# Performance work log

Hardware: AMD Instinct MI355X
Metric: run time of the kernel (lower is better)

Reference implementation:

```python
import jax, jax.numpy as jnp
import numpy as np

N_NODES = 50000
N_EDGES = 600000
D_IN = 128
D_HID = 128
N_IDX = 4096


def gcn_conv(x, W, b, edge_index, num_nodes):
    """PyG GCNConv: add self loops, symmetric deg normalization, scatter-add, bias."""
    h = x @ W  # [N, D_out]
    loop = jnp.arange(num_nodes, dtype=edge_index.dtype)
    src = jnp.concatenate([edge_index[0], loop])
    dst = jnp.concatenate([edge_index[1], loop])
    deg = jax.ops.segment_sum(jnp.ones_like(dst, dtype=h.dtype), dst, num_segments=num_nodes)
    dinv = jnp.where(deg > 0, jax.lax.rsqrt(jnp.maximum(deg, 1.0)), 0.0)
    norm = dinv[src] * dinv[dst]  # [E+N]
    msgs = h[src] * norm[:, None]
    out = jax.ops.segment_sum(msgs, dst, num_segments=num_nodes)
    return out + b


def setup_inputs() -> dict:
    key = jax.random.key(0)
    ks = jax.random.split(key, 18)
    d = {
        "x": jax.random.normal(ks[0], (N_NODES, D_IN), dtype=jnp.float32),
        "syntactic_edge_index": jax.random.randint(ks[1], (2, N_EDGES), 0, N_NODES, dtype=jnp.int32),
        "sequential_edge_index": jax.random.randint(ks[2], (2, N_EDGES), 0, N_NODES, dtype=jnp.int32),
        "semantic_edge_index": jax.random.randint(ks[3], (2, N_EDGES), 0, N_NODES, dtype=jnp.int32),
        "index": jax.random.randint(ks[4], (N_IDX,), 0, N_NODES, dtype=jnp.int32),
    }
    s = 1.0 / np.sqrt(D_IN)
    names = ["syn", "seq", "sem"]
    for i, n in enumerate(names):
        d[f"w1_{n}"] = jax.random.uniform(ks[5 + i], (D_IN, D_HID), jnp.float32, -s, s)
        d[f"b1_{n}"] = jnp.zeros((D_HID,), jnp.float32)
        d[f"w2_{n}"] = jax.random.uniform(ks[8 + i], (D_HID, D_HID), jnp.float32, -s, s)
        d[f"b2_{n}"] = jnp.zeros((D_HID,), jnp.float32)
    return d


def reference(x, syntactic_edge_index, sequential_edge_index, semantic_edge_index, index,
              w1_syn, b1_syn, w1_seq, b1_seq, w1_sem, b1_sem,
              w2_syn, b2_syn, w2_seq, b2_seq, w2_sem, b2_sem):
    n = x.shape[0]
    # layer 1: three parallel GCN branches + ReLU (dropout is identity in eval mode)
    a = jax.nn.relu(gcn_conv(x, w1_syn, b1_syn, syntactic_edge_index, n))
    b = jax.nn.relu(gcn_conv(x, w1_seq, b1_seq, sequential_edge_index, n))
    c = jax.nn.relu(gcn_conv(x, w1_sem, b1_sem, semantic_edge_index, n))
    h = jnp.maximum(jnp.maximum(a, b), c)
    # layer 2
    a2 = jax.nn.relu(gcn_conv(h, w2_syn, b2_syn, syntactic_edge_index, n))
    b2 = jax.nn.relu(gcn_conv(h, w2_seq, b2_seq, sequential_edge_index, n))
    c2 = jax.nn.relu(gcn_conv(h, w2_sem, b2_sem, semantic_edge_index, n))
    out = jnp.maximum(jnp.maximum(a2, b2), c2)
    return out[index]
```

## Files before the change

kernel.cpp:

```cpp
#include <hip/hip_runtime.h>
#include <hip/hip_fp16.h>

#define NN 50000
#define NE 600000
#define NG 3
#define D  128
#define NI 4096
#define BW 1024
#define NBUCK 49
#define EPT_BIN 16
#define EPB_BIN (256 * EPT_BIN)
#define NBLK_BIN ((NE + EPB_BIN - 1) / EPB_BIN)
#define XCVT_BLKS 3125
#define WCVT_BLKS 48
#define CNT_BLKS (NBLK_BIN * NG)

typedef _Float16 half8 __attribute__((ext_vector_type(8)));
typedef _Float16 half4v __attribute__((ext_vector_type(4)));
typedef float floatx4 __attribute__((ext_vector_type(4)));

static __device__ __forceinline__ float wextract(unsigned int v) {
  unsigned short u = (unsigned short)(v >> 16);
  _Float16 h;
  __builtin_memcpy(&h, &u, 2);
  return (float)h;
}

static __device__ __forceinline__ unsigned int packsw(int s, float w) {
  _Float16 h = (_Float16)w;
  unsigned short u;
  __builtin_memcpy(&u, &h, 2);
  return (unsigned int)s | ((unsigned int)u << 16);
}


__global__ __launch_bounds__(256) void prep_kernel(
    const float* __restrict__ x, __half* __restrict__ xh,
    const float* __restrict__ W0, const float* __restrict__ W1, const float* __restrict__ W2,
    const float* __restrict__ W3, const float* __restrict__ W4, const float* __restrict__ W5,
    __half* __restrict__ Wf,
    const int* __restrict__ e0, const int* __restrict__ e1, const int* __restrict__ e2,
    int* __restrict__ bucketCnt) {
  __shared__ int cnt[NBUCK];
  int blk = blockIdx.x;
  int tid = threadIdx.x;
  if (blk < XCVT_BLKS) {
    int i = blk * 256 + tid;
    size_t base = (size_t)i * 8;
    float4 v0 = *(const float4*)&x[base];
    float4 v1 = *(const float4*)&x[base + 4];
    half8 h;
    h[0] = (_Float16)v0.x; h[1] = (_Float16)v0.y; h[2] = (_Float16)v0.z; h[3] = (_Float16)v0.w;
    h[4] = (_Float16)v1.x; h[5] = (_Float16)v1.y; h[6] = (_Float16)v1.z; h[7] = (_Float16)v1.w;
    *(half8*)&xh[base] = h;
  } else if (blk < XCVT_BLKS + WCVT_BLKS) {
    const float* Wm[6] = {W0, W1, W2, W3, W4, W5};
    int t = (blk - XCVT_BLKS) * 256 + tid;
    int mat = t >> 11;
    int fr = (t >> 6) & 31;
    int lane = t & 63;
    int tt = fr >> 2, ks = fr & 3;
    int n = tt * 16 + (lane & 15);
    int kb = ks * 32 + (lane >> 4) * 8;
    const float* W = Wm[mat];
#pragma unroll
    for (int j = 0; j < 8; j++)
      Wf[(size_t)t * 8 + j] = __float2half(W[(kb + j) * 128 + n]);
  } else {
    int cb = blk - XCVT_BLKS - WCVT_BLKS;
    int g = cb / NBLK_BIN, eb = cb % NBLK_BIN;
    const int* ei = (g == 0) ? e0 : ((g == 1) ? e1 : e2);
    if (tid < NBUCK) cnt[tid] = 0;
    __syncthreads();
    int base = eb * EPB_BIN;
#pragma unroll
    for (int i = 0; i < EPT_BIN; i++) {
      int e = base + tid + i * 256;
      if (e < NE) atomicAdd(&cnt[ei[NE + e] >> 10], 1);
    }
    __syncthreads();
    if (tid < NBUCK) atomicAdd(&bucketCnt[g * NBUCK + tid], cnt[tid]);
  }
}

__global__ void bscan_kernel(const int* __restrict__ bucketCnt, int* __restrict__ bucketBase,
                             int* __restrict__ cursor, int* __restrict__ rp) {
  int g = threadIdx.x >> 6;
  int lane = threadIdx.x & 63;
  if (g >= NG) return;
  int v = (lane < NBUCK) ? bucketCnt[g * NBUCK + lane] : 0;
  int incl = v;
#pragma unroll
  for (int off = 1; off < 64; off <<= 1) {
    int t = __shfl_up(incl, off, 64);
    if (lane >= off) incl += t;
  }
  int ex = incl - v;
  if (lane < NBUCK) {
    bucketBase[g * NBUCK + lane] = ex;
    cursor[g * NBUCK + lane] = ex;
  }
  if (lane == 0) rp[g * (NN + 1) + NN] = NE;
}

__global__ __launch_bounds__(256) void bin_kernel(const int* __restrict__ e0,
    const int* __restrict__ e1, const int* __restrict__ e2,
    int* __restrict__ cursor, unsigned int* __restrict__ binned) {
  __shared__ int cnt[4][NBUCK];
  __shared__ int base[NBUCK];
  __shared__ int woff[4][NBUCK];
  int g = blockIdx.y;
  const int* ei = (g == 0) ? e0 : ((g == 1) ? e1 : e2);
  int tid = threadIdx.x;
  int wave = tid >> 6;
  if (tid < NBUCK) { cnt[0][tid] = 0; cnt[1][tid] = 0; cnt[2][tid] = 0; cnt[3][tid] = 0; }
  __syncthreads();
  int estart = blockIdx.x * EPB_BIN;
  int src[EPT_BIN], dst[EPT_BIN], rk[EPT_BIN];
#pragma unroll
  for (int i = 0; i < EPT_BIN; i++) {
    int e = estart + tid + i * 256;
    if (e < NE) {
      src[i] = ei[e];
      dst[i] = ei[NE + e];
      rk[i] = atomicAdd(&cnt[wave][dst[i] >> 10], 1);
    } else {
      rk[i] = -1;
    }
  }
  __syncthreads();
  if (tid < NBUCK) {
    int c0 = cnt[0][tid], c1 = cnt[1][tid], c2 = cnt[2][tid], c3 = cnt[3][tid];
    int total = c0 + c1 + c2 + c3;
    base[tid] = (total > 0) ? atomicAdd(&cursor[g * NBUCK + tid], total) : 0;
    woff[0][tid] = 0; woff[1][tid] = c0; woff[2][tid] = c0 + c1; woff[3][tid] = c0 + c1 + c2;
  }
  __syncthreads();
#pragma unroll
  for (int i = 0; i < EPT_BIN; i++) {
    if (rk[i] >= 0) {
      int b = dst[i] >> 10;
      binned[(size_t)g * NE + base[b] + woff[wave][b] + rk[i]] =
          (unsigned int)src[i] | ((unsigned int)dst[i] << 16);
    }
  }
}

__global__ __launch_bounds__(256) void csr_kernel(const unsigned int* __restrict__ binned,
    const int* __restrict__ bucketBase, const int* __restrict__ bucketCnt,
    int* __restrict__ rp, float* __restrict__ dinv) {
  __shared__ int deg[BW];
  __shared__ int wsum[4];
  int g = blockIdx.y, b = blockIdx.x;
  int tid = threadIdx.x;
  int node0 = b * BW;
  int bb = bucketBase[g * NBUCK + b];
  int total = bucketCnt[g * NBUCK + b];
  const unsigned int* bp = binned + (size_t)g * NE + bb;
  for (int i = tid; i < BW; i += 256) deg[i] = 0;
  __syncthreads();
  for (int e = tid; e < total; e += 256) {
    unsigned int p = bp[e];
    atomicAdd(&deg[(int)(p >> 16) - node0], 1);
  }
  __syncthreads();
  int d0 = deg[tid * 4], d1 = deg[tid * 4 + 1], d2 = deg[tid * 4 + 2], d3 = deg[tid * 4 + 3];
  int s = d0 + d1 + d2 + d3;
  int lane = tid & 63;
  int incl = s;
#pragma unroll
  for (int off = 1; off < 64; off <<= 1) {
    int n = __shfl_up(incl, off, 64);
    if (lane >= off) incl += n;
  }
  if (lane == 63) wsum[tid >> 6] = incl;
  __syncthreads();
  int wbase = 0;
#pragma unroll
  for (int w = 0; w < 4; w++)
    if (w < (tid >> 6)) wbase += wsum[w];
  int ex = wbase + incl - s;
  int exs[4] = {ex, ex + d0, ex + d0 + d1, ex + d0 + d1 + d2};
  int ds[4] = {d0, d1, d2, d3};
#pragma unroll
  for (int k = 0; k < 4; k++) {
    int node = node0 + tid * 4 + k;
    if (node < NN) {
      rp[g * (NN + 1) + node] = bb + exs[k];
      dinv[g * NN + node] = rsqrtf((float)ds[k] + 1.0f);
    }
  }
}

__global__ __launch_bounds__(256) void fillp_kernel(const unsigned int* __restrict__ binned,
    const int* __restrict__ bucketBase, const int* __restrict__ bucketCnt,
    const int* __restrict__ rp, const float* __restrict__ dinv,
    unsigned int* __restrict__ colp) {
  __shared__ int cur[BW];
  int g = blockIdx.y, b = blockIdx.x;
  int tid = threadIdx.x;
  int node0 = b * BW;
  int bb = bucketBase[g * NBUCK + b];
  int total = bucketCnt[g * NBUCK + b];
  const unsigned int* bp = binned + (size_t)g * NE + bb;
  for (int i = tid; i < BW; i += 256) {
    int node = node0 + i;
    cur[i] = (node < NN) ? rp[g * (NN + 1) + node] : 0;
  }
  __syncthreads();
  for (int e = tid; e < total; e += 256) {
    unsigned int p = bp[e];
    int srcid = (int)(p & 0xffffu);
    int r = atomicAdd(&cur[(int)(p >> 16) - node0], 1);
    colp[(size_t)g * NE + r] = packsw(srcid, dinv[g * NN + srcid]);
  }
}


__global__ __launch_bounds__(256) void aggb_kernel(
    const __half* __restrict__ srch, const int* __restrict__ rp,
    const unsigned int* __restrict__ colp, const float* __restrict__ dinv,
    const int* __restrict__ index, __half* __restrict__ tout, int nrows) {
  int b = blockIdx.y;
  int w = (blockIdx.x * 256 + threadIdx.x) >> 6;
  if (w >= nrows) return;
  int lane = threadIdx.x & 63;
  int sub = lane >> 5;
  int fl = lane & 31;
  int node = index ? index[w] : w;
  const _Float16* srcv = (const _Float16*)srch;
  half4v selfh = *(const half4v*)&srcv[(size_t)node * D + fl * 4];
  float di = dinv[b * NN + node];
  float a[4];
#pragma unroll
  for (int k = 0; k < 4; k++) a[k] = sub ? 0.f : di * (float)selfh[k];
  const int* rpb = rp + b * (NN + 1);
  int s = rpb[node], e = rpb[node + 1];
  int n = e - s;
  const unsigned int* cp = colp + (size_t)b * NE;
  unsigned int c = (lane < n) ? cp[s + lane] : 0u;
  int m = min(n, 64);
  for (int j = 0; j < m; j += 8) {
    half4v h[4];
    float wg[4];
#pragma unroll
    for (int u = 0; u < 4; u++) {
      unsigned int v = (unsigned int)__shfl((int)c, j + u * 2 + sub, 64);
      wg[u] = wextract(v);
      h[u] = *(const half4v*)&srcv[(size_t)(v & 0xffffu) * D + fl * 4];
    }
#pragma unroll
    for (int u = 0; u < 4; u++)
#pragma unroll
      for (int k = 0; k < 4; k++) a[k] = fmaf((float)h[u][k], wg[u], a[k]);
  }
  for (int q = s + 64; q < e; q += 64) {
    int nn = min(e - q, 64);
    unsigned int cc = (lane < nn) ? cp[q + lane] : 0u;
    for (int j = 0; j < nn; j += 2) {
      unsigned int v = (unsigned int)__shfl((int)cc, j + sub, 64);
      float wf = wextract(v);
      half4v hv = *(const half4v*)&srcv[(size_t)(v & 0xffffu) * D + fl * 4];
#pragma unroll
      for (int k = 0; k < 4; k++) a[k] = fmaf((float)hv[k], wf, a[k]);
    }
  }
#pragma unroll
  for (int k = 0; k < 4; k++) a[k] += __shfl_xor(a[k], 32, 64);
  if (sub == 0) {
    half4v o;
#pragma unroll
    for (int k = 0; k < 4; k++) o[k] = (_Float16)(di * a[k]);
    _Float16* tv = (_Float16*)tout;
    *(half4v*)&tv[(size_t)b * nrows * D + (size_t)w * D + fl * 4] = o;
  }
}


#define ALD 136

__global__ __launch_bounds__(256) void mmf_kernel(const __half* __restrict__ A,
    const __half* __restrict__ Wf,
    const float* __restrict__ B0, const float* __restrict__ B1, const float* __restrict__ B2,
    __half* __restrict__ outh, float* __restrict__ outf, int M) {
  __shared__ _Float16 As[128 * ALD];
  __shared__ _Float16 Ws[16384];
  const float* Bb[3] = {B0, B1, B2};
  const int tid = threadIdx.x;
  const int wave = tid >> 6, lane = tid & 63;
  const int wr = (wave >> 1) * 64, wc = (wave & 1) * 64;
  const int ln = lane & 15, quad = lane >> 4;
  const int row0 = blockIdx.x * 128;
  float om[4][4][4];

  for (int b = 0; b < 3; b++) {
    const __half* Wb = Wf + (size_t)b * 16384;
#pragma unroll
    for (int i = 0; i < 8; i++) {
      int id = tid + i * 256;
      *(half8*)&Ws[id * 8] = *(const half8*)&Wb[(size_t)id * 8];
    }
    const __half* Ab = A + (size_t)b * M * D;
#pragma unroll
    for (int i = 0; i < 8; i++) {
      int idx = tid + i * 256;
      int r = idx >> 4, c8 = idx & 15;
      int gr = row0 + r;
      gr = (gr < M) ? gr : (M - 1);
      half8 v = *(const half8*)&Ab[(size_t)gr * D + c8 * 8];
      *(half8*)&As[r * ALD + c8 * 8] = v;
    }
    __syncthreads();

    float bias[4];
#pragma unroll
    for (int ct = 0; ct < 4; ct++) bias[ct] = Bb[b][wc + ct * 16 + ln];
    floatx4 acc[4][4];
#pragma unroll
    for (int rt = 0; rt < 4; rt++)
#pragma unroll
      for (int ct = 0; ct < 4; ct++)
        acc[rt][ct] = (floatx4){bias[ct], bias[ct], bias[ct], bias[ct]};

#pragma unroll
    for (int ks = 0; ks < 4; ks++) {
      half8 av[4];
#pragma unroll
      for (int rt = 0; rt < 4; rt++)
        av[rt] = *(const half8*)&As[(wr + rt * 16 + ln) * ALD + ks * 32 + quad * 8];
#pragma unroll
      for (int ct = 0; ct < 4; ct++) {
        int tt = (wc >> 4) + ct;
        half8 bv = *(const half8*)&Ws[((tt * 4 + ks) * 64 + lane) * 8];
#pragma unroll
        for (int rt = 0; rt < 4; rt++)
          acc[rt][ct] = __builtin_amdgcn_mfma_f32_16x16x32_f16(av[rt], bv, acc[rt][ct], 0, 0, 0);
      }
    }
#pragma unroll
    for (int rt = 0; rt < 4; rt++)
#pragma unroll
      for (int ct = 0; ct < 4; ct++)
#pragma unroll
        for (int r = 0; r < 4; r++) {
          float v = fmaxf(acc[rt][ct][r], 0.f);
          om[rt][ct][r] = (b == 0) ? v : fmaxf(om[rt][ct][r], v);
        }
    __syncthreads();
  }
#pragma unroll
  for (int rt = 0; rt < 4; rt++) {
    int m = row0 + wr + rt * 16 + quad * 4;
#pragma unroll
    for (int r = 0; r < 4; r++) {
      if (m + r < M) {
#pragma unroll
        for (int ct = 0; ct < 4; ct++) {
          int n = wc + ct * 16 + ln;
          if (outh) outh[(size_t)(m + r) * D + n] = __float2half(om[rt][ct][r]);
          else      outf[(size_t)(m + r) * D + n] = om[rt][ct][r];
        }
      }
    }
  }
}


extern "C" void kernel_launch(void* const* d_in, const int* in_sizes, int n_in,
                              void* d_out, int out_size, void* d_ws, size_t ws_size,
                              hipStream_t stream) {
  const float* x = (const float*)d_in[0];
  const int* e0 = (const int*)d_in[1];
  const int* e1 = (const int*)d_in[2];
  const int* e2 = (const int*)d_in[3];
  const int* index = (const int*)d_in[4];
  const float* w1[3] = {(const float*)d_in[5], (const float*)d_in[9],  (const float*)d_in[13]};
  const float* b1[3] = {(const float*)d_in[6], (const float*)d_in[10], (const float*)d_in[14]};
  const float* w2[3] = {(const float*)d_in[7], (const float*)d_in[11], (const float*)d_in[15]};
  const float* b2[3] = {(const float*)d_in[8], (const float*)d_in[12], (const float*)d_in[16]};
  float* out = (float*)d_out;

  char* ws = (char*)d_ws;
  size_t o = 0;
  auto alloc = [&](size_t bytes) {
    o = (o + 255) & ~(size_t)255;
    void* p = ws + o;
    o += bytes;
    return p;
  };
  int*    rp     = (int*)alloc((size_t)NG * (NN + 1) * 4);
  unsigned int* colp = (unsigned int*)alloc((size_t)NG * NE * 4);
  float*  dinv   = (float*)alloc((size_t)NG * NN * 4);
  int*    bcnt   = (int*)alloc((size_t)NG * NBUCK * 4);
  int*    bbase  = (int*)alloc((size_t)NG * NBUCK * 4);
  int*    bcur   = (int*)alloc((size_t)NG * NBUCK * 4);
  __half* xh     = (__half*)alloc((size_t)NN * D * 2);
  __half* Wf     = (__half*)alloc((size_t)6 * 128 * 128 * 2);
  __half* t1     = (__half*)alloc((size_t)NG * NN * D * 2);
  __half* hacc   = (__half*)alloc((size_t)NN * D * 2);
  unsigned int* binned = (unsigned int*)t1;
  __half* t2     = t1;
  (void)ws_size; (void)in_sizes; (void)n_in; (void)out_size;

  hipMemsetAsync(bcnt, 0, (size_t)NG * NBUCK * 4, stream);
  prep_kernel<<<XCVT_BLKS + WCVT_BLKS + CNT_BLKS, 256, 0, stream>>>(
      x, xh, w1[0], w1[1], w1[2], w2[0], w2[1], w2[2], Wf, e0, e1, e2, bcnt);
  bscan_kernel<<<1, 192, 0, stream>>>(bcnt, bbase, bcur, rp);
  bin_kernel<<<dim3(NBLK_BIN, NG), 256, 0, stream>>>(e0, e1, e2, bcur, binned);
  csr_kernel<<<dim3(NBUCK, NG), 256, 0, stream>>>(binned, bbase, bcnt, rp, dinv);
  fillp_kernel<<<dim3(NBUCK, NG), 256, 0, stream>>>(binned, bbase, bcnt, rp, dinv, colp);

  aggb_kernel<<<dim3((NN * 64 + 255) / 256, NG), 256, 0, stream>>>(
      xh, rp, colp, dinv, nullptr, t1, NN);
  mmf_kernel<<<(NN + 127) / 128, 256, 0, stream>>>(t1, Wf, b1[0], b1[1], b1[2],
                                                   hacc, nullptr, NN);
  aggb_kernel<<<dim3((NI * 64 + 255) / 256, NG), 256, 0, stream>>>(
      hacc, rp, colp, dinv, index, t2, NI);
  mmf_kernel<<<(NI + 127) / 128, 256, 0, stream>>>(t2, Wf + (size_t)3 * 16384,
                                                   b2[0], b2[1], b2[2], nullptr, out, NI);
}
```

Baseline: 279.5 us.

## Aggregate four rows per wavefront with 16-lane groups and half8 loads

Reworks the gather-aggregation kernel so each 64-lane wavefront handles four destination rows, with 16 lanes per row each loading 8 fp16 features (16-byte loads) instead of two 32-lane halves per row with 8-byte loads. Neighbor indices are fetched 16 at a time per group and broadcast by shuffle, and the final cross-half reduction is removed. The intent is to improve memory-load width and cut per-row shuffle and reduction overhead for low-degree nodes (average degree around 12). The cost is divergence: each wavefront loops to the maximum degree of its four rows, and the launch grid shrinks accordingly.

Result: no change. 275.6 us (-1.4%).

```diff
diff --git a/kernel.cpp b/kernel.cpp
--- a/kernel.cpp
+++ b/kernel.cpp
@@ -222,57 +222,60 @@
     const unsigned int* __restrict__ colp, const float* __restrict__ dinv,
     const int* __restrict__ index, __half* __restrict__ tout, int nrows) {
   int b = blockIdx.y;
-  int w = (blockIdx.x * 256 + threadIdx.x) >> 6;
-  if (w >= nrows) return;
   int lane = threadIdx.x & 63;
-  int sub = lane >> 5;
-  int fl = lane & 31;
-  int node = index ? index[w] : w;
+  int grp = lane >> 4;
+  int l16 = lane & 15;
+  int gb = grp << 4;
+  int wv = (blockIdx.x * 256 + threadIdx.x) >> 6;
+  int w = wv * 4 + grp;
+  int valid = (w < nrows);
+  int wc = valid ? w : 0;
+  int node = index ? index[wc] : wc;
   const _Float16* srcv = (const _Float16*)srch;
-  half4v selfh = *(const half4v*)&srcv[(size_t)node * D + fl * 4];
+  const int* rpb = rp + b * (NN + 1);
+  int s = rpb[node];
+  int e = rpb[node + 1];
+  int n = valid ? (e - s) : 0;
   float di = dinv[b * NN + node];
-  float a[4];
-#pragma unroll
-  for (int k = 0; k < 4; k++) a[k] = sub ? 0.f : di * (float)selfh[k];
-  const int* rpb = rp + b * (NN + 1);
-  int s = rpb[node], e = rpb[node + 1];
-  int n = e - s;
+  half8 selfh = *(const half8*)&srcv[(size_t)node * D + l16 * 8];
+  float a[8];
+#pragma unroll
+  for (int k = 0; k < 8; k++) a[k] = di * (float)selfh[k];
+  int nmax = n;
+  nmax = max(nmax, __shfl_xor(nmax, 16, 64));
+  nmax = max(nmax, __shfl_xor(nmax, 32, 64));
   const unsigned int* cp = colp + (size_t)b * NE;
-  unsigned int c = (lane < n) ? cp[s + lane] : 0u;
-  int m = min(n, 64);
-  for (int j = 0; j < m; j += 8) {
-    half4v h[4];
-    float wg[4];
-#pragma unroll
-    for (int u = 0; u < 4; u++) {
-      unsigned int v = (unsigned int)__shfl((int)c, j + u * 2 + sub, 64);
-      wg[u] = wextract(v);
-      h[u] = *(const half4v*)&srcv[(size_t)(v & 0xffffu) * D + fl * 4];
-    }
-#pragma unroll
-    for (int u = 0; u < 4; u++)
-#pragma unroll
-      for (int k = 0; k < 4; k++) a[k] = fmaf((float)h[u][k], wg[u], a[k]);
-  }
-  for (int q = s + 64; q < e; q += 64) {
-    int nn = min(e - q, 64);
-    unsigned int cc = (lane < nn) ? cp[q + lane] : 0u;
-    for (int j = 0; j < nn; j += 2) {
-      unsigned int v = (unsigned int)__shfl((int)cc, j + sub, 64);
-      float wf = wextract(v);
-      half4v hv = *(const half4v*)&srcv[(size_t)(v & 0xffffu) * D + fl * 4];
-#pragma unroll
-      for (int k = 0; k < 4; k++) a[k] = fmaf((float)hv[k], wf, a[k]);
-    }
-  }
-#pragma unroll
-  for (int k = 0; k < 4; k++) a[k] += __shfl_xor(a[k], 32, 64);
-  if (sub == 0) {
-    half4v o;
-#pragma unroll
-    for (int k = 0; k < 4; k++) o[k] = (_Float16)(di * a[k]);
+  for (int j0 = 0; j0 < nmax; j0 += 16) {
+    unsigned int c = (j0 + l16 < n) ? cp[s + j0 + l16] : 0u;
+    int rem = nmax - j0;
+    rem = (rem > 16) ? 16 : rem;
+    for (int jj = 0; jj < rem; jj += 4) {
+      unsigned int v0 = (unsigned int)__shfl((int)c, gb + jj + 0, 64);
+      unsigned int v1 = (unsigned int)__shfl((int)c, gb + jj + 1, 64);
+      unsigned int v2 = (unsigned int)__shfl((int)c, gb + jj + 2, 64);
+      unsigned int v3 = (unsigned int)__shfl((int)c, gb + jj + 3, 64);
+      half8 h0 = *(const half8*)&srcv[(size_t)(v0 & 0xffffu) * D + l16 * 8];
+      half8 h1 = *(const half8*)&srcv[(size_t)(v1 & 0xffffu) * D + l16 * 8];
+      half8 h2 = *(const half8*)&srcv[(size_t)(v2 & 0xffffu) * D + l16 * 8];
+      half8 h3 = *(const half8*)&srcv[(size_t)(v3 & 0xffffu) * D + l16 * 8];
+      float w0 = wextract(v0), w1 = wextract(v1);
+      float w2 = wextract(v2), w3 = wextract(v3);
+#pragma unroll
+      for (int k = 0; k < 8; k++) a[k] = fmaf((float)h0[k], w0, a[k]);
+#pragma unroll
+      for (int k = 0; k < 8; k++) a[k] = fmaf((float)h1[k], w1, a[k]);
+#pragma unroll
+      for (int k = 0; k < 8; k++) a[k] = fmaf((float)h2[k], w2, a[k]);
+#pragma unroll
+      for (int k = 0; k < 8; k++) a[k] = fmaf((float)h3[k], w3, a[k]);
+    }
+  }
+  if (valid) {
+    half8 o;
+#pragma unroll
+    for (int k = 0; k < 8; k++) o[k] = (_Float16)(di * a[k]);
     _Float16* tv = (_Float16*)tout;
-    *(half4v*)&tv[(size_t)b * nrows * D + (size_t)w * D + fl * 4] = o;
+    *(half8*)&tv[(size_t)b * nrows * D + (size_t)w * D + l16 * 8] = o;
   }
 }
 
@@ -410,11 +413,11 @@
   csr_kernel<<<dim3(NBUCK, NG), 256, 0, stream>>>(binned, bbase, bcnt, rp, dinv);
   fillp_kernel<<<dim3(NBUCK, NG), 256, 0, stream>>>(binned, bbase, bcnt, rp, dinv, colp);
 
-  aggb_kernel<<<dim3((NN * 64 + 255) / 256, NG), 256, 0, stream>>>(
+  aggb_kernel<<<dim3((NN + 15) / 16, NG), 256, 0, stream>>>(
       xh, rp, colp, dinv, nullptr, t1, NN);
   mmf_kernel<<<(NN + 127) / 128, 256, 0, stream>>>(t1, Wf, b1[0], b1[1], b1[2],
                                                    hacc, nullptr, NN);
-  aggb_kernel<<<dim3((NI * 64 + 255) / 256, NG), 256, 0, stream>>>(
+  aggb_kernel<<<dim3((NI + 15) / 16, NG), 256, 0, stream>>>(
       hacc, rp, colp, dinv, index, t2, NI);
   mmf_kernel<<<(NI + 127) / 128, 256, 0, stream>>>(t2, Wf + (size_t)3 * 16384,
                                                    b2[0], b2[1], b2[2], nullptr, out, NI);
```
